# Optimization experiments

Hardware: AMD Instinct MI355X
Metric: run time of the kernel (lower is better)

## Reference

```python
import jax, jax.numpy as jnp
import numpy as np

N = 16384   # total gate nodes (64 graphs x 256 gates)
B = 64      # graphs in batch
E = 49152   # directed edges (avg in-degree 3)
Q = 32      # qubit_num
F = 256     # feat_dim
D = 2 * F   # node feature dim = 512
H = 2       # heads
A = 128     # action_num


def _gatv2(x, wl, wr, att, b, src, dst, n):
    # PyG GATv2Conv (concat=True, share_weights=False, negative_slope=0.2)
    h, c = att.shape
    xl = (x @ wl).reshape(n, h, c)   # source-side projection [N,H,C]
    xr = (x @ wr).reshape(n, h, c)   # target-side projection [N,H,C]
    e = jax.nn.leaky_relu(xl[src] + xr[dst], 0.2)       # [E,H,C]
    logit = jnp.einsum('ehc,hc->eh', e, att)             # [E,H]
    m = jax.ops.segment_max(logit, dst, num_segments=n)  # softmax over in-edges per target
    p = jnp.exp(logit - m[dst])
    den = jax.ops.segment_sum(p, dst, num_segments=n)
    alpha = p / den[dst]                                 # [E,H]
    out = jax.ops.segment_sum(alpha[:, :, None] * xl[src], dst, num_segments=n)
    return out.reshape(n, h * c) + b


def _forward(x, xt_w1, xt_b1, xt_w2, xt_b2,
             g0_wl, g0_wr, g0_att, g0_b,
             g1_wl, g1_wr, g1_att, g1_b,
             g2_wl, g2_wr, g2_att, g2_b,
             g3_wl, g3_wr, g3_att, g3_b,
             g4_wl, g4_wr, g4_att, g4_b,
             ln_w, ln_b, aggr_t,
             m_w1, m_b1, m_w2, m_b2, m_w3, m_b3,
             edge_index, batch):
    lr = lambda v: jax.nn.leaky_relu(v, 0.01)
    # x_trans: Linear -> LeakyReLU -> Linear, then fold qubit-pairs into one node
    h0 = lr(x @ xt_w1 + xt_b1) @ xt_w2 + xt_b2           # [2N, F]
    cx = h0.reshape(-1, D)                               # [N, 2F]
    n = cx.shape[0]
    # GATv2Conv default add_self_loops=True (inputs contain no self loops)
    sl = jnp.arange(n, dtype=edge_index.dtype)
    src = jnp.concatenate([edge_index[0], sl])
    dst = jnp.concatenate([edge_index[1], sl])
    res = cx
    h = lr(_gatv2(cx, g0_wl, g0_wr, g0_att, g0_b, src, dst, n))
    for wl_, wr_, att_, b_ in ((g1_wl, g1_wr, g1_att, g1_b),
                               (g2_wl, g2_wr, g2_att, g2_b),
                               (g3_wl, g3_wr, g3_att, g3_b)):
        h = lr(_gatv2(h, wl_, wr_, att_, b_, src, dst, n))
    h = lr(_gatv2(h, g4_wl, g4_wr, g4_att, g4_b, src, dst, n))
    h = h + res                                           # residual [N, 2F]
    # PyG LayerNorm(mode='graph'): normalize over nodes AND channels per graph
    cnt = jax.ops.segment_sum(jnp.ones((n,), h.dtype), batch, num_segments=B)
    norm = cnt * h.shape[1]
    mean = jax.ops.segment_sum(h.sum(-1), batch, num_segments=B) / norm
    hc = h - mean[batch][:, None]
    var = jax.ops.segment_sum((hc * hc).sum(-1), batch, num_segments=B) / norm
    h = hc / jnp.sqrt(var + 1e-5)[batch][:, None] * ln_w + ln_b
    # SoftmaxAggregation(learn=True): channel-wise softmax over nodes per graph
    logit = h * aggr_t
    mg = jax.ops.segment_max(logit, batch, num_segments=B)
    p = jnp.exp(logit - mg[batch])
    den = jax.ops.segment_sum(p, batch, num_segments=B)
    g = jax.ops.segment_sum((p / den[batch]) * h, batch, num_segments=B)  # [B, 2F]
    # head MLP 512->384->256->128
    o = lr(g @ m_w1 + m_b1)
    o = lr(o @ m_w2 + m_b2)
    return o @ m_w3 + m_b3


def setup_inputs() -> dict:
    key = jax.random.key(0)
    ks = iter(jax.random.split(key, 64))
    def rn(shp, s=0.05):
        return jax.random.normal(next(ks), shp, jnp.float32) * s
    d = {}
    d['x'] = jax.random.normal(next(ks), (2 * N, Q), jnp.float32)
    src = jax.random.randint(next(ks), (E,), 0, N, jnp.int32)
    off = jax.random.randint(next(ks), (E,), 1, N, jnp.int32)
    d['edge_index'] = jnp.stack([src, (src + off) % N])  # no self loops
    d['batch'] = jnp.arange(N, dtype=jnp.int32) // (N // B)
    d['xt_w1'] = rn((Q, F)); d['xt_b1'] = rn((F,))
    d['xt_w2'] = rn((F, F)); d['xt_b2'] = rn((F,))
    d['g0_wl'] = rn((D, H * D)); d['g0_wr'] = rn((D, H * D))
    d['g0_att'] = rn((H, D));    d['g0_b'] = rn((H * D,))
    for i in (1, 2, 3):
        d[f'g{i}_wl'] = rn((H * D, H * D)); d[f'g{i}_wr'] = rn((H * D, H * D))
        d[f'g{i}_att'] = rn((H, D));        d[f'g{i}_b'] = rn((H * D,))
    d['g4_wl'] = rn((H * D, D)); d['g4_wr'] = rn((H * D, D))
    d['g4_att'] = rn((1, D));    d['g4_b'] = rn((D,))
    d['ln_w'] = jnp.ones((D,), jnp.float32); d['ln_b'] = jnp.zeros((D,), jnp.float32)
    d['aggr_t'] = jnp.array(1.0, jnp.float32)
    d['m_w1'] = rn((D, 384)); d['m_b1'] = rn((384,))
    d['m_w2'] = rn((384, 256)); d['m_b2'] = rn((256,))
    d['m_w3'] = rn((256, A)); d['m_b3'] = rn((A,))
    return d


def reference(x, edge_index, batch, xt_w1, xt_b1, xt_w2, xt_b2,
              g0_wl, g0_wr, g0_att, g0_b,
              g1_wl, g1_wr, g1_att, g1_b,
              g2_wl, g2_wr, g2_att, g2_b,
              g3_wl, g3_wr, g3_att, g3_b,
              g4_wl, g4_wr, g4_att, g4_b,
              ln_w, ln_b, aggr_t,
              m_w1, m_b1, m_w2, m_b2, m_w3, m_b3):
    return _forward(x, xt_w1, xt_b1, xt_w2, xt_b2,
                    g0_wl, g0_wr, g0_att, g0_b,
                    g1_wl, g1_wr, g1_att, g1_b,
                    g2_wl, g2_wr, g2_att, g2_b,
                    g3_wl, g3_wr, g3_att, g3_b,
                    g4_wl, g4_wr, g4_att, g4_b,
                    ln_w, ln_b, aggr_t,
                    m_w1, m_b1, m_w2, m_b2, m_w3, m_b3,
                    edge_index, batch)
```

## Files before the change

kernel.cpp:

```cpp
#include <hip/hip_runtime.h>
#include <hip/hip_bf16.h>

typedef __hip_bfloat16 bf16;

#define NN 16384
#define BBG 64
#define EE 49152
#define ET (EE + NN)
#define DD 512
#define NG (NN / BBG)
#define RS1024 1152
#define RS512  640

__device__ __forceinline__ float b2f(bf16 v) { return __bfloat162float(v); }
__device__ __forceinline__ bf16 f2b(float v) { return __float2bfloat16(v); }
__device__ __forceinline__ float sb2f(short s) {
    unsigned u = ((unsigned)(unsigned short)s) << 16;
    return __builtin_bit_cast(float, u);
}
__device__ __forceinline__ short f2bs(float v) {
    bf16 b = f2b(v);
    return __builtin_bit_cast(short, b);
}
__device__ __forceinline__ int clampi(int v, int lo, int hi)
{
    return v < lo ? lo : (v > hi ? hi : v);
}

__device__ __forceinline__ unsigned char enc_e4m3(float y)
{
    unsigned b = __builtin_bit_cast(unsigned, y);
    unsigned s = (b >> 31) << 7;
    float a = fabsf(y);
    unsigned ab = b & 0x7fffffffu;
    unsigned rb = ab + (1u << 19);
    int e = (int)(rb >> 23) - 120;
    unsigned m = (rb >> 20) & 7u;
    unsigned qn = (unsigned)(e << 3) | m;
    if (qn > 126u) qn = 126u;
    unsigned qd = (unsigned)__float2int_rn(a * 512.f);
    unsigned q = (a < 0.015625f) ? qd : qn;
    return (unsigned char)(q | s);
}
__device__ __forceinline__ float dec_e4m3(unsigned q)
{
    unsigned e = (q >> 3) & 15u, m = q & 7u;
    float nrm = __builtin_bit_cast(float, ((e + 120u) << 23) | (m << 20));
    float dnm = (float)m * 0.001953125f;
    float v = e ? nrm : dnm;
    return (q & 128u) ? -v : v;
}

typedef __attribute__((ext_vector_type(8))) short bf16x8;
typedef __attribute__((ext_vector_type(4))) float f32x4;

#define AS1 __attribute__((address_space(1)))
#define AS3 __attribute__((address_space(3)))

__global__ __launch_bounds__(256) void gemm_mfma_bt(
    const bf16* __restrict__ A, const bf16* __restrict__ Bt,
    const float* __restrict__ bias, bf16* __restrict__ Cb,
    int M, int N, int K, float slope, int has_act)
{
    __shared__ bf16 As[128 * 32];
    __shared__ bf16 Bs[128 * 32];
    const int tid = threadIdx.x;
    const int w = tid >> 6;
    const int l = tid & 63;
    const int bm = blockIdx.y * 128;
    const int bn = blockIdx.x * 128;
    const int wrow = (w >> 1) * 64;
    const int wcol = (w & 1) * 64;
    const int quad = l >> 4;
    const int c16 = l & 15;

    const int lrow = l >> 2;
    const int lchunk = l & 3;
    const bf16* Ag = A + (size_t)(bm + w * 16 + lrow) * K + lchunk * 8;
    const bf16* Bg = Bt + (size_t)(bn + w * 16 + lrow) * K + lchunk * 8;
    char* AsB = (char*)As;
    char* BsB = (char*)Bs;

    f32x4 acc[4][4] = {};

    for (int k0 = 0; k0 < K; k0 += 32) {
        __builtin_amdgcn_global_load_lds((const AS1 void*)(Ag + k0),
            (AS3 void*)(AsB + w * 1024), 16, 0, 0);
        __builtin_amdgcn_global_load_lds((const AS1 void*)(Ag + (size_t)64 * K + k0),
            (AS3 void*)(AsB + 4096 + w * 1024), 16, 0, 0);
        __builtin_amdgcn_global_load_lds((const AS1 void*)(Bg + k0),
            (AS3 void*)(BsB + w * 1024), 16, 0, 0);
        __builtin_amdgcn_global_load_lds((const AS1 void*)(Bg + (size_t)64 * K + k0),
            (AS3 void*)(BsB + 4096 + w * 1024), 16, 0, 0);
        __syncthreads();

        bf16x8 a[4], b[4];
#pragma unroll
        for (int i = 0; i < 4; i++) {
            int ra = wrow + i * 16 + c16;
            a[i] = *(const bf16x8*)(AsB + ra * 64 + quad * 16);
            int rb = wcol + i * 16 + c16;
            b[i] = *(const bf16x8*)(BsB + rb * 64 + quad * 16);
        }
#pragma unroll
        for (int i = 0; i < 4; i++)
#pragma unroll
            for (int j = 0; j < 4; j++)
                acc[i][j] = __builtin_amdgcn_mfma_f32_16x16x32_bf16(
                    a[i], b[j], acc[i][j], 0, 0, 0);
        __syncthreads();
    }

#pragma unroll
    for (int i = 0; i < 4; i++) {
#pragma unroll
        for (int j = 0; j < 4; j++) {
            int col = bn + wcol + j * 16 + c16;
            float bv = bias ? bias[col] : 0.f;
#pragma unroll
            for (int r = 0; r < 4; r++) {
                int row = bm + wrow + i * 16 + quad * 4 + r;
                float v = acc[i][j][r] + bv;
                if (has_act) v = (v >= 0.f) ? v : v * slope;
                Cb[(size_t)row * N + col] = f2b(v);
            }
        }
    }
}

__global__ __launch_bounds__(256) void gemm_mfma_dual(
    const bf16* __restrict__ A, const bf16* __restrict__ Bt,
    bf16* __restrict__ X0, bf16* __restrict__ X1,
    int M, int K, int HC)
{
    __shared__ bf16 As[128 * 32];
    __shared__ bf16 Bs[128 * 32];
    const int tid = threadIdx.x;
    const int w = tid >> 6;
    const int l = tid & 63;
    const int bm = blockIdx.y * 128;
    const int bn = blockIdx.x * 128;
    const int wrow = (w >> 1) * 64;
    const int wcol = (w & 1) * 64;
    const int quad = l >> 4;
    const int c16 = l & 15;

    const int lrow = l >> 2;
    const int lchunk = l & 3;
    const bf16* Ag = A + (size_t)(bm + w * 16 + lrow) * K + lchunk * 8;
    const bf16* Bg = Bt + (size_t)(bn + w * 16 + lrow) * K + lchunk * 8;
    char* AsB = (char*)As;
    char* BsB = (char*)Bs;

    f32x4 acc[4][4] = {};

    for (int k0 = 0; k0 < K; k0 += 32) {
        __builtin_amdgcn_global_load_lds((const AS1 void*)(Ag + k0),
            (AS3 void*)(AsB + w * 1024), 16, 0, 0);
        __builtin_amdgcn_global_load_lds((const AS1 void*)(Ag + (size_t)64 * K + k0),
            (AS3 void*)(AsB + 4096 + w * 1024), 16, 0, 0);
        __builtin_amdgcn_global_load_lds((const AS1 void*)(Bg + k0),
            (AS3 void*)(BsB + w * 1024), 16, 0, 0);
        __builtin_amdgcn_global_load_lds((const AS1 void*)(Bg + (size_t)64 * K + k0),
            (AS3 void*)(BsB + 4096 + w * 1024), 16, 0, 0);
        __syncthreads();

        bf16x8 a[4], b[4];
#pragma unroll
        for (int i = 0; i < 4; i++) {
            int ra = wrow + i * 16 + c16;
            a[i] = *(const bf16x8*)(AsB + ra * 64 + quad * 16);
            int rb = wcol + i * 16 + c16;
            b[i] = *(const bf16x8*)(BsB + rb * 64 + quad * 16);
        }
#pragma unroll
        for (int i = 0; i < 4; i++)
#pragma unroll
            for (int j = 0; j < 4; j++)
                acc[i][j] = __builtin_amdgcn_mfma_f32_16x16x32_bf16(
                    a[i], b[j], acc[i][j], 0, 0, 0);
        __syncthreads();
    }

#pragma unroll
    for (int i = 0; i < 4; i++) {
#pragma unroll
        for (int j = 0; j < 4; j++) {
            int col = bn + wcol + j * 16 + c16;
            bf16* dst = (col < HC) ? (X0 + col) : (X1 + col - HC);
#pragma unroll
            for (int r = 0; r < 4; r++) {
                int row = bm + wrow + i * 16 + quad * 4 + r;
                dst[(size_t)row * HC] = f2b(acc[i][j][r]);
            }
        }
    }
}

__global__ __launch_bounds__(256, 4) void quant1024(
    const bf16* __restrict__ xl, unsigned char* __restrict__ xp)
{
    const int n = blockIdx.x * 4 + (threadIdx.x >> 6);
    const int lane = threadIdx.x & 63;
    const bf16* rp = xl + (size_t)n * 1024 + lane * 16;
    bf16x8 v0 = *(const bf16x8*)(rp);
    bf16x8 v1 = *(const bf16x8*)(rp + 8);
    float x[16];
#pragma unroll
    for (int k = 0; k < 8; k++) { x[k] = sb2f(v0[k]); x[8 + k] = sb2f(v1[k]); }
    float mx = 0.f;
#pragma unroll
    for (int k = 0; k < 16; k++) mx = fmaxf(mx, fabsf(x[k]));
    float sc = b2f(f2b(fmaxf(mx, 1e-20f) * (1.f / 448.f)));
    float isc = 1.f / sc;
    uint4 q;
    unsigned* qw = (unsigned*)&q;
#pragma unroll
    for (int w = 0; w < 4; w++) {
        unsigned pk = 0;
#pragma unroll
        for (int b = 0; b < 4; b++)
            pk |= ((unsigned)enc_e4m3(x[w * 4 + b] * isc)) << (b * 8);
        qw[w] = pk;
    }
    unsigned char* row = xp + (size_t)n * RS1024;
    *(uint4*)(row + 128 + lane * 16) = q;
    ((bf16*)row)[lane] = f2b(sc);
}

__global__ __launch_bounds__(256, 4) void quant512(
    const bf16* __restrict__ xl, unsigned char* __restrict__ xp)
{
    const int n = blockIdx.x * 4 + (threadIdx.x >> 6);
    const int lane = threadIdx.x & 63;
    bf16x8 v0 = *(const bf16x8*)(xl + (size_t)n * 512 + lane * 8);
    float x[8];
#pragma unroll
    for (int k = 0; k < 8; k++) x[k] = sb2f(v0[k]);
    float mx = 0.f;
#pragma unroll
    for (int k = 0; k < 8; k++) mx = fmaxf(mx, fabsf(x[k]));
    float sc = b2f(f2b(fmaxf(mx, 1e-20f) * (1.f / 448.f)));
    float isc = 1.f / sc;
    uint2 q;
    unsigned* qw = (unsigned*)&q;
#pragma unroll
    for (int w = 0; w < 2; w++) {
        unsigned pk = 0;
#pragma unroll
        for (int b = 0; b < 4; b++)
            pk |= ((unsigned)enc_e4m3(x[w * 4 + b] * isc)) << (b * 8);
        qw[w] = pk;
    }
    unsigned char* row = xp + (size_t)n * RS512;
    *(uint2*)(row + 128 + lane * 8) = q;
    ((bf16*)row)[lane] = f2b(sc);
}

__global__ __launch_bounds__(256) void gemm_f32(
    const float* __restrict__ A, const float* __restrict__ W,
    const float* __restrict__ bias, float* __restrict__ C,
    int M, int N, int K, float slope, int has_act)
{
    const int BK = 16;
    __shared__ float Asm[BK][64 + 1];
    __shared__ float Wsm[BK][64 + 1];
    int tid = threadIdx.x;
    int bm = blockIdx.y * 64;
    int bn = blockIdx.x * 64;
    int tr = tid >> 4;
    int tc = tid & 15;
    float acc[4][4] = {};

    for (int k0 = 0; k0 < K; k0 += BK) {
        {
            int col = tid & 15;
            int row = tid >> 4;
#pragma unroll
            for (int p = 0; p < 4; p++) {
                int r = row + p * 16;
                Asm[col][r] = A[(size_t)(bm + r) * K + k0 + col];
            }
        }
        {
            int wc = tid & 63;
            int wr = tid >> 6;
#pragma unroll
            for (int p = 0; p < 4; p++) {
                int r = wr + p * 4;
                Wsm[r][wc] = W[(size_t)(k0 + r) * N + bn + wc];
            }
        }
        __syncthreads();
#pragma unroll
        for (int kk = 0; kk < BK; kk++) {
            float a[4], w[4];
#pragma unroll
            for (int i = 0; i < 4; i++) a[i] = Asm[kk][tr * 4 + i];
#pragma unroll
            for (int j = 0; j < 4; j++) w[j] = Wsm[kk][tc * 4 + j];
#pragma unroll
            for (int i = 0; i < 4; i++)
#pragma unroll
                for (int j = 0; j < 4; j++)
                    acc[i][j] += a[i] * w[j];
        }
        __syncthreads();
    }
#pragma unroll
    for (int i = 0; i < 4; i++) {
        int r = bm + tr * 4 + i;
#pragma unroll
        for (int j = 0; j < 4; j++) {
            int cn = bn + tc * 4 + j;
            float v = acc[i][j];
            if (bias) v += bias[cn];
            if (has_act) v = (v >= 0.f) ? v : v * slope;
            C[(size_t)r * N + cn] = v;
        }
    }
}

struct TPackAll {
    const float* in[12];
    bf16* out[12];
    int R[12], C[12];
};

__global__ __launch_bounds__(256) void transpose_batch(TPackAll pk)
{
    int z = blockIdx.z;
    int R = pk.R[z], C = pk.C[z];
    int c0 = blockIdx.x * 32;
    int r0 = blockIdx.y * 32;
    if (c0 >= C || r0 >= R) return;
    const float* in = pk.in[z];
    bf16* out = pk.out[z];
    __shared__ float tile[32][33];
    int tx = threadIdx.x & 31;
    int ty = threadIdx.x >> 5;
#pragma unroll
    for (int k = 0; k < 4; k++) {
        int r = ty + k * 8;
        tile[r][tx] = in[(size_t)(r0 + r) * C + c0 + tx];
    }
    __syncthreads();
#pragma unroll
    for (int k = 0; k < 4; k++) {
        int rr = ty + k * 8;
        out[(size_t)(c0 + rr) * R + r0 + tx] = f2b(tile[tx][rr]);
    }
}

__global__ void f2b_vec(const float* __restrict__ in, bf16* __restrict__ out, int n)
{
    int i = blockIdx.x * 256 + threadIdx.x;
    if (i < n) out[i] = f2b(in[i]);
}

__global__ void fill_csr(const int* __restrict__ ei, int* __restrict__ cur,
                         int* __restrict__ csrc)
{
    int e = blockIdx.x * 256 + threadIdx.x;
    if (e >= ET) return;
    int s, d;
    if (e < EE) { s = ei[e]; d = ei[EE + e]; } else { s = d = e - EE; }
    s = clampi(s, 0, NN - 1);
    d = clampi(d, 0, NN - 1);
    int pos = atomicAdd(&cur[d], 1);
    if (pos < 64) csrc[d * 64 + pos] = s;
}

__global__ __launch_bounds__(256, 4) void gat_q(
    const unsigned char* __restrict__ xp, const bf16* __restrict__ xr,
    const float* __restrict__ att, const float* __restrict__ bias,
    const int* __restrict__ cur, const int* __restrict__ csrc,
    bf16* __restrict__ out_b)
{
    constexpr int HC = 1024, CPL = 16;
    const int tid = threadIdx.x;
    const int w = tid >> 6;
    const int lane = tid & 63;
    const int n = blockIdx.x * 4 + w;
    const int c0 = lane * CPL;

    int deg = clampi(cur[n], 1, 64);
    int my_src = clampi(csrc[n * 64 + lane], 0, NN - 1);

    float av[CPL], rv[CPL];
    {
        bf16x8 r0 = *(const bf16x8*)(xr + (size_t)n * HC + c0);
        bf16x8 r1 = *(const bf16x8*)(xr + (size_t)n * HC + c0 + 8);
#pragma unroll
        for (int k = 0; k < 8; k++) { rv[k] = sb2f(r0[k]); rv[8 + k] = sb2f(r1[k]); }
#pragma unroll
        for (int k = 0; k < CPL; k++) av[k] = att[c0 + k];
    }

    float m = -1e30f, den = 0.f;
    float acc[CPL];
#pragma unroll
    for (int k = 0; k < CPL; k++) acc[k] = 0.f;

    auto loadrow = [&](int i, uint4& q, float& sc) {
        int s = __shfl(my_src, i);
        const unsigned char* row = xp + (size_t)s * RS1024;
        sc = b2f(*(const bf16*)(row + lane * 2));
        q = *(const uint4*)(row + 128 + lane * 16);
    };
    auto process = [&](const uint4& q, float sc) {
        float x[CPL];
        const unsigned* qw = (const unsigned*)&q;
#pragma unroll
        for (int k = 0; k < CPL; k++)
            x[k] = dec_e4m3((qw[k >> 2] >> ((k & 3) * 8)) & 255u) * sc;
        float part = 0.f;
#pragma unroll
        for (int k = 0; k < CPL; k++) {
            float u = x[k] + rv[k];
            u = (u >= 0.f) ? u : 0.2f * u;
            part = fmaf(av[k], u, part);
        }
#pragma unroll
        for (int msk = 16; msk; msk >>= 1) part += __shfl_xor(part, msk);
        float lg = part;
        float mn = fmaxf(m, lg);
        float r = __expf(m - mn);
        float pi = __expf(lg - mn);
        m = mn;
        den = den * r + pi;
#pragma unroll
        for (int k = 0; k < CPL; k++) acc[k] = fmaf(acc[k], r, pi * x[k]);
    };

    uint4 cq, q1, q2, qn;
    float cs, s1, s2, sn;
    loadrow(0, cq, cs);
    if (deg > 1) loadrow(1, q1, s1);
    if (deg > 2) loadrow(2, q2, s2);
    for (int i = 0; i < deg; i++) {
        if (i + 3 < deg) loadrow(i + 3, qn, sn);
        process(cq, cs);
        cq = q1; cs = s1; q1 = q2; s1 = s2; q2 = qn; s2 = sn;
    }

    float inv = 1.f / den;
    bf16x8 ov0, ov1;
#pragma unroll
    for (int k = 0; k < 8; k++) {
        float v = fmaf(acc[k], inv, bias[c0 + k]);
        v = (v >= 0.f) ? v : 0.01f * v;
        ov0[k] = f2bs(v);
        float v2 = fmaf(acc[8 + k], inv, bias[c0 + 8 + k]);
        v2 = (v2 >= 0.f) ? v2 : 0.01f * v2;
        ov1[k] = f2bs(v2);
    }
    *(bf16x8*)(out_b + (size_t)n * HC + c0) = ov0;
    *(bf16x8*)(out_b + (size_t)n * HC + c0 + 8) = ov1;
}

__global__ __launch_bounds__(256, 4) void gat_q512(
    const unsigned char* __restrict__ xp, const bf16* __restrict__ xr,
    const float* __restrict__ att, const float* __restrict__ bias,
    const int* __restrict__ cur, const int* __restrict__ csrc,
    const bf16* __restrict__ res, bf16* __restrict__ out_b,
    float* __restrict__ lnsums)
{
    constexpr int HC = 512, CPL = 8;
    const int tid = threadIdx.x;
    const int w = tid >> 6;
    const int lane = tid & 63;
    const int n = blockIdx.x * 4 + w;
    const int c0 = lane * CPL;

    int deg = clampi(cur[n], 1, 64);
    int my_src = clampi(csrc[n * 64 + lane], 0, NN - 1);

    float av[CPL], rv[CPL];
    {
        bf16x8 rp = *(const bf16x8*)(xr + (size_t)n * HC + c0);
#pragma unroll
        for (int k = 0; k < CPL; k++) {
            rv[k] = sb2f(rp[k]);
            av[k] = att[c0 + k];
        }
    }

    float m = -1e30f, den = 0.f;
    float acc[CPL];
#pragma unroll
    for (int k = 0; k < CPL; k++) acc[k] = 0.f;

    auto loadrow = [&](int i, uint2& q, float& sc) {
        int s = __shfl(my_src, i);
        const unsigned char* row = xp + (size_t)s * RS512;
        sc = b2f(*(const bf16*)(row + lane * 2));
        q = *(const uint2*)(row + 128 + lane * 8);
    };
    auto process = [&](const uint2& q, float sc) {
        float x[CPL];
        const unsigned* qw = (const unsigned*)&q;
#pragma unroll
        for (int k = 0; k < CPL; k++)
            x[k] = dec_e4m3((qw[k >> 2] >> ((k & 3) * 8)) & 255u) * sc;
        float part = 0.f;
#pragma unroll
        for (int k = 0; k < CPL; k++) {
            float u = x[k] + rv[k];
            u = (u >= 0.f) ? u : 0.2f * u;
            part = fmaf(av[k], u, part);
        }
#pragma unroll
        for (int msk = 32; msk; msk >>= 1) part += __shfl_xor(part, msk);
        float lg = part;
        float mn = fmaxf(m, lg);
        float r = __expf(m - mn);
        float pi = __expf(lg - mn);
        m = mn;
        den = den * r + pi;
#pragma unroll
        for (int k = 0; k < CPL; k++) acc[k] = fmaf(acc[k], r, pi * x[k]);
    };

    uint2 cq, q1, q2, qn;
    float cs, s1, s2, sn;
    loadrow(0, cq, cs);
    if (deg > 1) loadrow(1, q1, s1);
    if (deg > 2) loadrow(2, q2, s2);
    for (int i = 0; i < deg; i++) {
        if (i + 3 < deg) loadrow(i + 3, qn, sn);
        process(cq, cs);
        cq = q1; cs = s1; q1 = q2; s1 = s2; q2 = qn; s2 = sn;
    }

    float inv = 1.f / den;
    float ls = 0.f, ls2 = 0.f;
    float vals[CPL];
#pragma unroll
    for (int k = 0; k < CPL; k++) {
        float v = fmaf(acc[k], inv, bias[c0 + k]);
        v = (v >= 0.f) ? v : 0.01f * v;
        vals[k] = v;
    }
    {
        bf16x8 rr = *(const bf16x8*)(res + (size_t)n * HC + c0);
#pragma unroll
        for (int k = 0; k < CPL; k++) {
            vals[k] += sb2f(rr[k]);
            ls += vals[k];
            ls2 += vals[k] * vals[k];
        }
    }
    bf16x8 ov;
#pragma unroll
    for (int k = 0; k < 8; k++) ov[k] = f2bs(vals[k]);
    *(bf16x8*)(out_b + (size_t)n * HC + c0) = ov;

#pragma unroll
    for (int msk = 32; msk; msk >>= 1) {
        ls += __shfl_xor(ls, msk);
        ls2 += __shfl_xor(ls2, msk);
    }
    if (lane == 0) {
        int g = n >> 8;
        atomicAdd(&lnsums[g], ls);
        atomicAdd(&lnsums[BBG + g], ls2);
    }
}

__global__ __launch_bounds__(256) void aggr_partial(
    const bf16* __restrict__ h, const float* __restrict__ lnsums,
    const float* __restrict__ lnw, const float* __restrict__ lnb,
    const float* __restrict__ t_, float* __restrict__ pm,
    float* __restrict__ pd, float* __restrict__ pa)
{
    int g = blockIdx.x, ch = blockIdx.y, nk = blockIdx.z;
    int tid = threadIdx.x;
    int c = ch * 256 + tid;
    const float tot = (float)(NG * DD);
    float S = lnsums[g], S2 = lnsums[BBG + g];
    float mu = S / tot;
    float iv = rsqrtf(fmaxf(S2 / tot - mu * mu, 0.f) + 1e-5f);
    float w = lnw[c], b = lnb[c], t = t_[0];
    size_t base = (size_t)g * NG * DD + (size_t)nk * 32 * DD + c;
    float m = -1e30f, den = 0.f, acc = 0.f;
    for (int i = 0; i < 32; i++) {
        float hn = (b2f(h[base + (size_t)i * DD]) - mu) * iv * w + b;
        float lg = hn * t;
        if (lg > m) {
            float r = __expf(m - lg);
            den *= r; acc *= r; m = lg;
        }
        float p = __expf(lg - m);
        den += p; acc += p * hn;
    }
    size_t idx = (((size_t)g * 2 + ch) * 8 + nk) * 256 + tid;
    pm[idx] = m; pd[idx] = den; pa[idx] = acc;
}

__global__ __launch_bounds__(256) void aggr_combine(
    const float* __restrict__ pm, const float* __restrict__ pd,
    const float* __restrict__ pa, float* __restrict__ gout)
{
    int g = blockIdx.x, ch = blockIdx.y;
    int tid = threadIdx.x;
    size_t base = (((size_t)g * 2 + ch) * 8) * 256 + tid;
    float m = -1e30f;
#pragma unroll
    for (int k = 0; k < 8; k++) m = fmaxf(m, pm[base + k * 256]);
    float den = 0.f, acc = 0.f;
#pragma unroll
    for (int k = 0; k < 8; k++) {
        float r = __expf(pm[base + k * 256] - m);
        den += pd[base + k * 256] * r;
        acc += pa[base + k * 256] * r;
    }
    gout[(size_t)g * DD + ch * 256 + tid] = acc / den;
}

extern "C" void kernel_launch(void* const* d_in, const int* in_sizes, int n_in,
                              void* d_out, int out_size, void* d_ws, size_t ws_size,
                              hipStream_t stream)
{
    const float* x      = (const float*)d_in[0];
    const int*   ei     = (const int*)d_in[1];
    const float* xt_w1  = (const float*)d_in[3];
    const float* xt_b1  = (const float*)d_in[4];
    const float* xt_w2  = (const float*)d_in[5];
    const float* xt_b2  = (const float*)d_in[6];
    const float* ln_w   = (const float*)d_in[27];
    const float* ln_b   = (const float*)d_in[28];
    const float* aggr_t = (const float*)d_in[29];
    const float* m_w1   = (const float*)d_in[30];
    const float* m_b1   = (const float*)d_in[31];
    const float* m_w2   = (const float*)d_in[32];
    const float* m_b2   = (const float*)d_in[33];
    const float* m_w3   = (const float*)d_in[34];
    const float* m_b3   = (const float*)d_in[35];
    float* out = (float*)d_out;

    char* p = (char*)d_ws;
    auto take = [&](size_t bytes) {
        char* r = p;
        p += (bytes + 255) & ~(size_t)255;
        return r;
    };
    int* i_cur     = (int*)take((size_t)NN * 4);
    int* i_src     = (int*)take((size_t)NN * 64 * 4);
    float* f_sums  = (float*)take((size_t)2 * BBG * 4);
    float* f_pm    = (float*)take((size_t)BBG * 2 * 8 * 256 * 4);
    float* f_pd    = (float*)take((size_t)BBG * 2 * 8 * 256 * 4);
    float* f_pa    = (float*)take((size_t)BBG * 2 * 8 * 256 * 4);
    float* b_g     = (float*)take((size_t)BBG * DD * 4);
    float* b_m1    = (float*)take((size_t)BBG * 384 * 4);
    float* b_m2    = (float*)take((size_t)BBG * 256 * 4);
    bf16* b_resb   = (bf16*)take((size_t)NN * DD * 2);
    bf16* b_h      = (bf16*)take((size_t)NN * DD * 2);
    bf16* b_hb     = (bf16*)take((size_t)NN * 1024 * 2);
    bf16* b_xlb    = (bf16*)take((size_t)NN * 1024 * 2);
    bf16* b_xrb    = (bf16*)take((size_t)NN * 1024 * 2);
    unsigned char* b_xp = (unsigned char*)take((size_t)NN * RS1024);
    bf16* b_xb     = (bf16*)take((size_t)2 * NN * 32 * 2);
    bf16* b_wcat   = (bf16*)take((size_t)8 * 1024 * 1024 * 2);
    bf16* b_w1b    = (bf16*)take((size_t)32 * 256 * 2);
    bf16* b_w2b    = (bf16*)take((size_t)256 * 256 * 2);
    bf16* b_t1b = b_hb;

    size_t woff[5];
    {
        size_t o = 0;
        for (int L = 0; L < 5; L++) {
            int Fin = (L == 0) ? 512 : 1024;
            int HC  = (L == 4) ? 512 : 1024;
            woff[L] = o;
            o += (size_t)2 * HC * Fin;
        }
    }

    dim3 blk(256);

    hipMemsetAsync(i_cur, 0, (size_t)NN * 4, stream);
    hipMemsetAsync(f_sums, 0, (size_t)2 * BBG * 4, stream);
    fill_csr<<<ET / 256, blk, 0, stream>>>(ei, i_cur, i_src);

    f2b_vec<<<(2 * NN * 32 + 255) / 256, blk, 0, stream>>>(x, b_xb, 2 * NN * 32);
    {
        TPackAll pk;
        pk.in[0] = xt_w1; pk.out[0] = b_w1b; pk.R[0] = 32;  pk.C[0] = 256;
        pk.in[1] = xt_w2; pk.out[1] = b_w2b; pk.R[1] = 256; pk.C[1] = 256;
        for (int L = 0; L < 5; L++) {
            int Fin = (L == 0) ? 512 : 1024;
            int HC  = (L == 4) ? 512 : 1024;
            pk.in[2 + 2 * L] = (const float*)d_in[7 + 4 * L];
            pk.out[2 + 2 * L] = b_wcat + woff[L];
            pk.R[2 + 2 * L] = Fin; pk.C[2 + 2 * L] = HC;
            pk.in[3 + 2 * L] = (const float*)d_in[8 + 4 * L];
            pk.out[3 + 2 * L] = b_wcat + woff[L] + (size_t)HC * Fin;
            pk.R[3 + 2 * L] = Fin; pk.C[3 + 2 * L] = HC;
        }
        transpose_batch<<<dim3(32, 32, 12), blk, 0, stream>>>(pk);
    }

    gemm_mfma_bt<<<dim3(256 / 128, 32768 / 128), blk, 0, stream>>>(
        b_xb, b_w1b, xt_b1, b_t1b, 32768, 256, 32, 0.01f, 1);
    gemm_mfma_bt<<<dim3(256 / 128, 32768 / 128), blk, 0, stream>>>(
        b_t1b, b_w2b, xt_b2, b_resb, 32768, 256, 256, 0.f, 0);

    for (int L = 0; L < 5; L++) {
        const float* att = (const float*)d_in[9 + 4 * L];
        const float* gb  = (const float*)d_in[10 + 4 * L];
        int Fin = (L == 0) ? 512 : 1024;
        int HC  = (L == 4) ? 512 : 1024;
        const bf16* hin = (L == 0) ? b_resb : b_hb;

        gemm_mfma_dual<<<dim3(2 * HC / 128, NN / 128), blk, 0, stream>>>(
            hin, b_wcat + woff[L], b_xlb, b_xrb, NN, Fin, HC);
        if (L < 4) {
            quant1024<<<NN / 4, blk, 0, stream>>>(b_xlb, b_xp);
            gat_q<<<NN / 4, blk, 0, stream>>>(
                b_xp, b_xrb, att, gb, i_cur, i_src, b_hb);
        } else {
            quant512<<<NN / 4, blk, 0, stream>>>(b_xlb, b_xp);
            gat_q512<<<NN / 4, blk, 0, stream>>>(
                b_xp, b_xrb, att, gb, i_cur, i_src, b_resb, b_h, f_sums);
        }
    }

    aggr_partial<<<dim3(BBG, 2, 8), blk, 0, stream>>>(
        b_h, f_sums, ln_w, ln_b, aggr_t, f_pm, f_pd, f_pa);
    aggr_combine<<<dim3(BBG, 2), blk, 0, stream>>>(f_pm, f_pd, f_pa, b_g);

    gemm_f32<<<dim3(384 / 64, 1), blk, 0, stream>>>(
        b_g, m_w1, m_b1, b_m1, 64, 384, 512, 0.01f, 1);
    gemm_f32<<<dim3(256 / 64, 1), blk, 0, stream>>>(
        b_m1, m_w2, m_b2, b_m2, 64, 256, 384, 0.01f, 1);
    gemm_f32<<<dim3(128 / 64, 1), blk, 0, stream>>>(
        b_m2, m_w3, m_b3, out, 64, 128, 256, 0.f, 0);
}
```

Measured before the change: 1.063 ms.

## Remap GEMM blocks per XCD and process GAT nodes in degree-sorted order

The dual-projection GEMM now runs on a 1D grid. Each block index is remapped so that consecutive blocks on the same XCD (id & 7) share a contiguous band of 16 row-tiles, which is meant to improve L2 reuse of the A operand. A new single-block kernel counting-sorts nodes by in-degree, and the GAT aggregation kernels process nodes in that order, so the four waves in a block have similar edge counts and less load imbalance. The cost is an extra serial kernel launch, and output rows are written in a scattered order instead of contiguously.

Measured after the change: 1.044 ms. No clear change (-1.8%).

```diff
diff --git a/kernel.cpp b/kernel.cpp
--- a/kernel.cpp
+++ b/kernel.cpp
@@ -131,15 +131,22 @@
 __global__ __launch_bounds__(256) void gemm_mfma_dual(
     const bf16* __restrict__ A, const bf16* __restrict__ Bt,
     bf16* __restrict__ X0, bf16* __restrict__ X1,
-    int M, int K, int HC)
-{
+    int K, int HC)
+{
+    const int NBX = HC >> 6;
+    const int id = blockIdx.x;
+    const int xcd = id & 7;
+    const int s = id >> 3;
+    const int by = xcd * 16 + s / NBX;
+    const int bx = s % NBX;
+
     __shared__ bf16 As[128 * 32];
     __shared__ bf16 Bs[128 * 32];
     const int tid = threadIdx.x;
     const int w = tid >> 6;
     const int l = tid & 63;
-    const int bm = blockIdx.y * 128;
-    const int bn = blockIdx.x * 128;
+    const int bm = by * 128;
+    const int bn = bx * 128;
     const int wrow = (w >> 1) * 64;
     const int wcol = (w & 1) * 64;
     const int quad = l >> 4;
@@ -371,17 +378,39 @@
     if (pos < 64) csrc[d * 64 + pos] = s;
 }
 
+__global__ __launch_bounds__(256) void sort_nodes(
+    const int* __restrict__ cur, int* __restrict__ order)
+{
+    __shared__ int cnt[65], base[65];
+    int tid = threadIdx.x;
+    if (tid < 65) cnt[tid] = 0;
+    __syncthreads();
+    for (int n = tid; n < NN; n += 256)
+        atomicAdd(&cnt[clampi(cur[n], 0, 64)], 1);
+    __syncthreads();
+    if (tid == 0) {
+        int a = 0;
+        for (int d = 0; d <= 64; d++) { base[d] = a; a += cnt[d]; }
+    }
+    __syncthreads();
+    for (int n = tid; n < NN; n += 256) {
+        int d = clampi(cur[n], 0, 64);
+        int pos = atomicAdd(&base[d], 1);
+        order[clampi(pos, 0, NN - 1)] = n;
+    }
+}
+
 __global__ __launch_bounds__(256, 4) void gat_q(
     const unsigned char* __restrict__ xp, const bf16* __restrict__ xr,
     const float* __restrict__ att, const float* __restrict__ bias,
     const int* __restrict__ cur, const int* __restrict__ csrc,
-    bf16* __restrict__ out_b)
+    const int* __restrict__ order, bf16* __restrict__ out_b)
 {
     constexpr int HC = 1024, CPL = 16;
     const int tid = threadIdx.x;
     const int w = tid >> 6;
     const int lane = tid & 63;
-    const int n = blockIdx.x * 4 + w;
+    const int n = clampi(order[blockIdx.x * 4 + w], 0, NN - 1);
     const int c0 = lane * CPL;
 
     int deg = clampi(cur[n], 1, 64);
@@ -463,14 +492,14 @@
     const unsigned char* __restrict__ xp, const bf16* __restrict__ xr,
     const float* __restrict__ att, const float* __restrict__ bias,
     const int* __restrict__ cur, const int* __restrict__ csrc,
-    const bf16* __restrict__ res, bf16* __restrict__ out_b,
-    float* __restrict__ lnsums)
+    const int* __restrict__ order, const bf16* __restrict__ res,
+    bf16* __restrict__ out_b, float* __restrict__ lnsums)
 {
     constexpr int HC = 512, CPL = 8;
     const int tid = threadIdx.x;
     const int w = tid >> 6;
     const int lane = tid & 63;
-    const int n = blockIdx.x * 4 + w;
+    const int n = clampi(order[blockIdx.x * 4 + w], 0, NN - 1);
     const int c0 = lane * CPL;
 
     int deg = clampi(cur[n], 1, 64);
@@ -647,6 +676,7 @@
     };
     int* i_cur     = (int*)take((size_t)NN * 4);
     int* i_src     = (int*)take((size_t)NN * 64 * 4);
+    int* i_ord     = (int*)take((size_t)NN * 4);
     float* f_sums  = (float*)take((size_t)2 * BBG * 4);
     float* f_pm    = (float*)take((size_t)BBG * 2 * 8 * 256 * 4);
     float* f_pd    = (float*)take((size_t)BBG * 2 * 8 * 256 * 4);
@@ -682,6 +712,7 @@
     hipMemsetAsync(i_cur, 0, (size_t)NN * 4, stream);
     hipMemsetAsync(f_sums, 0, (size_t)2 * BBG * 4, stream);
     fill_csr<<<ET / 256, blk, 0, stream>>>(ei, i_cur, i_src);
+    sort_nodes<<<1, blk, 0, stream>>>(i_cur, i_ord);
 
     f2b_vec<<<(2 * NN * 32 + 255) / 256, blk, 0, stream>>>(x, b_xb, 2 * NN * 32);
     {
@@ -712,17 +743,18 @@
         int Fin = (L == 0) ? 512 : 1024;
         int HC  = (L == 4) ? 512 : 1024;
         const bf16* hin = (L == 0) ? b_resb : b_hb;
-
-        gemm_mfma_dual<<<dim3(2 * HC / 128, NN / 128), blk, 0, stream>>>(
-            hin, b_wcat + woff[L], b_xlb, b_xrb, NN, Fin, HC);
+        int nblocks = (HC >> 6) * (NN / 128);
+
+        gemm_mfma_dual<<<dim3(nblocks), blk, 0, stream>>>(
+            hin, b_wcat + woff[L], b_xlb, b_xrb, Fin, HC);
         if (L < 4) {
             quant1024<<<NN / 4, blk, 0, stream>>>(b_xlb, b_xp);
             gat_q<<<NN / 4, blk, 0, stream>>>(
-                b_xp, b_xrb, att, gb, i_cur, i_src, b_hb);
+                b_xp, b_xrb, att, gb, i_cur, i_src, i_ord, b_hb);
         } else {
             quant512<<<NN / 4, blk, 0, stream>>>(b_xlb, b_xp);
             gat_q512<<<NN / 4, blk, 0, stream>>>(
-                b_xp, b_xrb, att, gb, i_cur, i_src, b_resb, b_h, f_sums);
+                b_xp, b_xrb, att, gb, i_cur, i_src, i_ord, b_resb, b_h, f_sums);
         }
     }
 
```
